# Performance work log

Measured on AMD Instinct MI355X. Metric: run time of the kernel, lower is better.

The kernel has to match this reference:

```python
import jax, jax.numpy as jnp
import numpy as np

N = 512   # speakers
M = 64    # samples per speaker
D = 768   # embedding dim
EPS = 1e-8  # torch F.cosine_similarity eps


def setup_inputs() -> dict:
    key = jax.random.key(0)
    k1, = jax.random.split(key, 1)
    speaker_vectors = jax.random.normal(k1, (N * M, D), dtype=jnp.float32)
    w = jnp.asarray(10.0, dtype=jnp.float32)
    b = jnp.asarray(-5.0, dtype=jnp.float32)
    return {"speaker_vectors": speaker_vectors, "w": w, "b": b}


def _cosine(a, b):
    # torch F.cosine_similarity: a.b / (max(|a|,eps) * max(|b|,eps)), over last dim
    na = jnp.maximum(jnp.linalg.norm(a, axis=-1), EPS)
    nb = jnp.maximum(jnp.linalg.norm(b, axis=-1), EPS)
    return jnp.sum(a * b, axis=-1) / (na * nb)


def reference(speaker_vectors, w, b):
    x = speaker_vectors.reshape(N, M, D)            # [N, M, D]
    sums = x.sum(axis=1)                            # [N, D]
    centroids = sums / M                            # [N, D]
    excl = (sums[:, None, :] - x) / (M - 1)         # exclusive centroids [N, M, D]

    # cosine sim of every centroid against every sample: [N_centroid, N_spk, M]
    xn = jnp.maximum(jnp.linalg.norm(x, axis=-1), EPS)          # [N, M]
    cn = jnp.maximum(jnp.linalg.norm(centroids, axis=-1), EPS)  # [N]
    dots = jnp.einsum('nd,imd->nim', centroids, x)              # [N, N, M]
    S = w * (dots / (cn[:, None, None] * xn[None])) + b         # [N, N, M]

    # same-speaker entries use the leave-one-out centroid
    S_same = w * _cosine(excl, x) + b               # [N, M]
    idx = jnp.arange(N)
    S = S.at[idx, idx].set(S_same)                  # overwrite diagonal block

    # L_j = -S_same_j + log sum_n exp(S[n, j])
    L = -S_same + jax.scipy.special.logsumexp(S, axis=0)  # [N, M]
    return L.sum()
```

## Files before the change

kernel.cpp:

```cpp
#include <hip/hip_runtime.h>
#include <hip/hip_bf16.h>
#include <math.h>

#define EPS 1e-8f

typedef __attribute__((ext_vector_type(2))) unsigned long ulongx2;
typedef __attribute__((ext_vector_type(4))) float floatx4;
typedef unsigned char uchar_t;

#define GPTR(p) ((const __attribute__((address_space(1))) void*)(p))
#define LPTR(p) ((__attribute__((address_space(3))) void*)(p))

__device__ __forceinline__ unsigned int pk4(float a, float b, float c, float d) {
  int v = __builtin_amdgcn_cvt_pk_fp8_f32(a, b, 0, false);
  v = __builtin_amdgcn_cvt_pk_fp8_f32(c, d, v, true);
  return (unsigned int)v;
}

__global__ __launch_bounds__(256) void kA(const float* __restrict__ x,
    uchar_t* __restrict__ xbf8fm, float* __restrict__ sums_f32,
    float* __restrict__ ss, float* __restrict__ rcn,
    float* __restrict__ xx, float* __restrict__ rxn,
    const float* __restrict__ wp) {
  const int n = blockIdx.x;
  const int t = threadIdx.x;
  const int wv = t >> 6, l = t & 63;
  __shared__ uchar_t xs[4][16][776];
  __shared__ float csum[4][768];
  float4 cs0 = {0,0,0,0}, cs1 = {0,0,0,0}, cs2 = {0,0,0,0};

  for (int r = 0; r < 16; ++r) {
    const int row = wv * 16 + r;
    const size_t base = ((size_t)n * 64 + row) * 768;
    const float* rp = x + base;
    float4 v0 = *(const float4*)(rp + l * 4);
    float4 v1 = *(const float4*)(rp + l * 4 + 256);
    float4 v2 = *(const float4*)(rp + l * 4 + 512);
    *(unsigned int*)&xs[wv][r][l * 4]       = pk4(v0.x, v0.y, v0.z, v0.w);
    *(unsigned int*)&xs[wv][r][l * 4 + 256] = pk4(v1.x, v1.y, v1.z, v1.w);
    *(unsigned int*)&xs[wv][r][l * 4 + 512] = pk4(v2.x, v2.y, v2.z, v2.w);
    float rq = v0.x*v0.x + v0.y*v0.y + v0.z*v0.z + v0.w*v0.w
             + v1.x*v1.x + v1.y*v1.y + v1.z*v1.z + v1.w*v1.w
             + v2.x*v2.x + v2.y*v2.y + v2.z*v2.z + v2.w*v2.w;
    for (int o = 32; o; o >>= 1) rq += __shfl_xor(rq, o, 64);
    if (l == 0) {
      const int j = n * 64 + row;
      xx[j] = rq;
      rxn[j] = 1.0f / fmaxf(sqrtf(rq), EPS);
    }
    cs0.x += v0.x; cs0.y += v0.y; cs0.z += v0.z; cs0.w += v0.w;
    cs1.x += v1.x; cs1.y += v1.y; cs1.z += v1.z; cs1.w += v1.w;
    cs2.x += v2.x; cs2.y += v2.y; cs2.z += v2.z; cs2.w += v2.w;
  }
  *(float4*)&csum[wv][l * 4]       = cs0;
  *(float4*)&csum[wv][l * 4 + 256] = cs1;
  *(float4*)&csum[wv][l * 4 + 512] = cs2;
  __syncthreads();

  float lss = 0.f;
#pragma unroll
  for (int q = 0; q < 3; ++q) {
    const int c = t + q * 256;
    const float s = csum[0][c] + csum[1][c] + csum[2][c] + csum[3][c];
    sums_f32[(size_t)n * 768 + c] = s;
    lss += s * s;
  }
  for (int o = 32; o; o >>= 1) lss += __shfl_xor(lss, o, 64);
  __syncthreads();
  if (l == 0) csum[1][wv] = lss;
  __syncthreads();
  if (t == 0) {
    const float v = csum[1][0] + csum[1][1] + csum[1][2] + csum[1][3];
    ss[n] = v;
    rcn[n] = (*wp) / fmaxf(sqrtf(v), 64.f * EPS);
  }

  {
    const int g = n * 4 + wv;
#pragma unroll
    for (int ks = 0; ks < 12; ++ks) {
      const uchar_t* sp = &xs[wv][l & 15][ks * 64 + (l >> 4) * 8];
      uint2 lo = *(const uint2*)sp;
      uint2 hi = *(const uint2*)(sp + 32);
      uint4 outv = {lo.x, lo.y, hi.x, hi.y};
      *(uint4*)(xbf8fm + (size_t)((g * 12 + ks) * 64 + l) * 16) = outv;
    }
  }
}

__global__ __launch_bounds__(256) void kA2(const float* __restrict__ sums_f32,
    uchar_t* __restrict__ sums8fm) {
  const int g = blockIdx.x;
  const int wv = threadIdx.x >> 6, l = threadIdx.x & 63;
#pragma unroll
  for (int ksi = 0; ksi < 3; ++ksi) {
    const int ks = wv * 3 + ksi;
    const float* sp = sums_f32 + (size_t)(g * 16 + (l & 15)) * 768
                      + ks * 64 + (l >> 4) * 8;
    float4 a0 = *(const float4*)sp;
    float4 a1 = *(const float4*)(sp + 4);
    float4 b0 = *(const float4*)(sp + 32);
    float4 b1 = *(const float4*)(sp + 36);
    uint4 outv = { pk4(a0.x, a0.y, a0.z, a0.w), pk4(a1.x, a1.y, a1.z, a1.w),
                   pk4(b0.x, b0.y, b0.z, b0.w), pk4(b1.x, b1.y, b1.z, b1.w) };
    *(uint4*)(sums8fm + (size_t)((g * 12 + ks) * 64 + l) * 16) = outv;
  }
}

__global__ __launch_bounds__(512, 2) void kC(const uchar_t* __restrict__ xbf8fm,
    const uchar_t* __restrict__ sums8fm, const float* __restrict__ rcn,
    const float* __restrict__ rxn, float* __restrict__ colsum,
    float* __restrict__ sdiag_dot, const float* __restrict__ bp) {
  __shared__ uchar_t lds[4][32768];
  const int b = blockIdx.x;
  const int xcd = b & 7;
  const int inner = b >> 3;
  const int nt = inner & 1;
  const int jt = xcd + ((inner >> 1) << 3);
  const int n0 = nt * 256, j0 = jt * 256;
  const int t = threadIdx.x, wv = t >> 6, l = t & 63;
  const int wm = wv >> 2, wj = wv & 3;
  const int gA0 = n0 / 16, gB0 = j0 / 16;

#define STAGE(KS_, BUF_) {                                                     \
    const int fb0_ = wv * 2, fb1_ = wv * 2 + 1;                                \
    __builtin_amdgcn_global_load_lds(                                          \
        GPTR(sums8fm + (size_t)(((gA0 + fb0_) * 12 + (KS_)) * 64 + l) * 16),   \
        LPTR(&lds[BUF_][fb0_ * 1024]), 16, 0, 0);                              \
    __builtin_amdgcn_global_load_lds(                                          \
        GPTR(sums8fm + (size_t)(((gA0 + fb1_) * 12 + (KS_)) * 64 + l) * 16),   \
        LPTR(&lds[BUF_][fb1_ * 1024]), 16, 0, 0);                              \
    __builtin_amdgcn_global_load_lds(                                          \
        GPTR(xbf8fm + (size_t)(((gB0 + fb0_) * 12 + (KS_)) * 64 + l) * 16),    \
        LPTR(&lds[BUF_][16384 + fb0_ * 1024]), 16, 0, 0);                      \
    __builtin_amdgcn_global_load_lds(                                          \
        GPTR(xbf8fm + (size_t)(((gB0 + fb1_) * 12 + (KS_)) * 64 + l) * 16),    \
        LPTR(&lds[BUF_][16384 + fb1_ * 1024]), 16, 0, 0);                      \
  }

  floatx4 acc[8][4];
#pragma unroll
  for (int mi = 0; mi < 8; ++mi)
#pragma unroll
    for (int ni = 0; ni < 4; ++ni) acc[mi][ni] = (floatx4){0.f, 0.f, 0.f, 0.f};

  STAGE(0, 0)
  STAGE(1, 1)
  STAGE(2, 2)

  for (int kb = 0; kb < 12; ++kb) {
    if (kb < 10)       { asm volatile("s_waitcnt vmcnt(8)" ::: "memory"); }
    else if (kb == 10) { asm volatile("s_waitcnt vmcnt(4)" ::: "memory"); }
    else               { asm volatile("s_waitcnt vmcnt(0)" ::: "memory"); }
    __builtin_amdgcn_s_barrier();
    __builtin_amdgcn_sched_barrier(0);
    const int cb = kb & 3, sb = (kb + 3) & 3;

    ulongx2 af[8], bf[4];
#pragma unroll
    for (int ni = 0; ni < 4; ++ni)
      bf[ni] = *(const ulongx2*)&lds[cb][16384 + (wj * 4 + ni) * 1024 + l * 16];
#pragma unroll
    for (int mi = 0; mi < 8; ++mi)
      af[mi] = *(const ulongx2*)&lds[cb][(wm * 8 + mi) * 1024 + l * 16];
    if (kb + 3 < 12) STAGE(kb + 3, sb)
    __builtin_amdgcn_s_setprio(1);
#pragma unroll
    for (int mi = 0; mi < 8; ++mi)
#pragma unroll
      for (int ni = 0; ni < 4; ++ni) {
        acc[mi][ni] = __builtin_amdgcn_mfma_f32_16x16x32_fp8_fp8(
            (long)af[mi].x, (long)bf[ni].x, acc[mi][ni], 0, 0, 0);
        acc[mi][ni] = __builtin_amdgcn_mfma_f32_16x16x32_fp8_fp8(
            (long)af[mi].y, (long)bf[ni].y, acc[mi][ni], 0, 0, 0);
      }
    __builtin_amdgcn_s_setprio(0);
  }

  const float bb = *bp;
  float rxv[4], p[4] = {0.f, 0.f, 0.f, 0.f};
#pragma unroll
  for (int ni = 0; ni < 4; ++ni)
    rxv[ni] = rxn[j0 + wj * 64 + ni * 16 + (l & 15)];
  const bool diagblk = (nt == (jt >> 6));

#pragma unroll
  for (int mi = 0; mi < 8; ++mi) {
    float4 rr = *(const float4*)&rcn[n0 + wm * 128 + mi * 16 + ((l >> 4) << 2)];
    const float rc[4] = {rr.x, rr.y, rr.z, rr.w};
#pragma unroll
    for (int ni = 0; ni < 4; ++ni) {
      floatx4 a = acc[mi][ni];
#pragma unroll
      for (int q = 0; q < 4; ++q)
        p[ni] += __expf(a[q] * rc[q] * rxv[ni] + bb);
      if (diagblk) {
        const int jg = j0 + wj * 64 + ni * 16 + (l & 15);
#pragma unroll
        for (int q = 0; q < 4; ++q) {
          const int mg = n0 + wm * 128 + mi * 16 + ((l >> 4) << 2) + q;
          if (mg == (jg >> 6)) sdiag_dot[jg] = a[q];
        }
      }
    }
  }
#pragma unroll
  for (int ni = 0; ni < 4; ++ni) {
    p[ni] += __shfl_xor(p[ni], 16, 64);
    p[ni] += __shfl_xor(p[ni], 32, 64);
  }
  if (l < 16) {
#pragma unroll
    for (int ni = 0; ni < 4; ++ni)
      atomicAdd(&colsum[j0 + wj * 64 + ni * 16 + l], p[ni]);
  }
}

__global__ __launch_bounds__(256) void kD(const float* __restrict__ colsum,
    const float* __restrict__ sdiag_dot, const float* __restrict__ xx,
    const float* __restrict__ ss, const float* __restrict__ rcn,
    const float* __restrict__ wp, const float* __restrict__ bp,
    float* __restrict__ out) {
  const int j = blockIdx.x * 256 + threadIdx.x;
  const int i = j >> 6;
  const float ww = *wp, bb = *bp;
  const float sx = sdiag_dot[j];
  const float xxv = xx[j];
  const float xn = fmaxf(sqrtf(xxv), EPS);
  const float rx = 1.0f / xn;
  const float sd = sx * rcn[i] * rx + bb;
  const float exn = sqrtf(fmaxf(ss[i] - 2.f * sx + xxv, 0.f)) * (1.f / 63.f);
  const float edot = (sx - xxv) * (1.f / 63.f);
  const float sm = ww * edot / (fmaxf(exn, EPS) * xn) + bb;
  const float tot = colsum[j] - __expf(sd) + __expf(sm);
  float L = -sm + logf(fmaxf(tot, 1e-30f));
  for (int o = 32; o; o >>= 1) L += __shfl_xor(L, o, 64);
  __shared__ float red[4];
  if ((threadIdx.x & 63) == 0) red[threadIdx.x >> 6] = L;
  __syncthreads();
  if (threadIdx.x == 0) atomicAdd(out, red[0] + red[1] + red[2] + red[3]);
}

extern "C" void kernel_launch(void* const* d_in, const int* in_sizes, int n_in,
                              void* d_out, int out_size, void* d_ws, size_t ws_size,
                              hipStream_t stream) {
  const float* x  = (const float*)d_in[0];
  const float* wp = (const float*)d_in[1];
  const float* bp = (const float*)d_in[2];
  float* out = (float*)d_out;

  float* fws = (float*)d_ws;
  float* ss        = fws;
  float* rcn       = fws + 512;
  float* xx        = fws + 1024;
  float* rxn       = fws + 33792;
  float* colsum    = fws + 66560;
  float* sdiag_dot = fws + 99328;
  float* sums_f32  = fws + 132096;
  uchar_t* sums8fm = (uchar_t*)(fws + 525312);
  uchar_t* xbf8fm  = (uchar_t*)(fws + 623616);

  hipMemsetAsync(colsum, 0, 32768 * sizeof(float), stream);
  hipMemsetAsync(out, 0, sizeof(float), stream);

  kA<<<512, 256, 0, stream>>>(x, xbf8fm, sums_f32, ss, rcn, xx, rxn, wp);
  kA2<<<32, 256, 0, stream>>>(sums_f32, sums8fm);
  kC<<<256, 512, 0, stream>>>(xbf8fm, sums8fm, rcn, rxn, colsum, sdiag_dot, bp);
  kD<<<128, 256, 0, stream>>>(colsum, sdiag_dot, xx, ss, rcn, wp, bp, out);
}
```

Before: 58.38 us.

## Split kA into 16-row blocks with atomic centroid sums; move norms to kA2

kA now launches one block per 16-sample group (2048 blocks) instead of one per speaker (512). Each block accumulates its partial speaker sums into a zeroed sums buffer with float atomics. The centroid squared-norm and scale computation moves into kA2, which now reads the completed sums. This is meant to raise occupancy and bandwidth use in the memory-bound conversion pass. The cost is an extra memset, 4-way atomic contention per element, and non-deterministic summation order.

```diff
diff --git a/kernel.cpp b/kernel.cpp
--- a/kernel.cpp
+++ b/kernel.cpp
@@ -19,32 +19,32 @@
 
 __global__ __launch_bounds__(256) void kA(const float* __restrict__ x,
     uchar_t* __restrict__ xbf8fm, float* __restrict__ sums_f32,
-    float* __restrict__ ss, float* __restrict__ rcn,
-    float* __restrict__ xx, float* __restrict__ rxn,
-    const float* __restrict__ wp) {
-  const int n = blockIdx.x;
+    float* __restrict__ xx, float* __restrict__ rxn) {
+  const int g = blockIdx.x;
+  const int n = g >> 2;
   const int t = threadIdx.x;
   const int wv = t >> 6, l = t & 63;
-  __shared__ uchar_t xs[4][16][776];
+  __shared__ uchar_t xs[16][776];
   __shared__ float csum[4][768];
   float4 cs0 = {0,0,0,0}, cs1 = {0,0,0,0}, cs2 = {0,0,0,0};
 
-  for (int r = 0; r < 16; ++r) {
-    const int row = wv * 16 + r;
-    const size_t base = ((size_t)n * 64 + row) * 768;
+#pragma unroll
+  for (int rr = 0; rr < 4; ++rr) {
+    const int r = wv * 4 + rr;
+    const size_t base = ((size_t)g * 16 + r) * 768;
     const float* rp = x + base;
     float4 v0 = *(const float4*)(rp + l * 4);
     float4 v1 = *(const float4*)(rp + l * 4 + 256);
     float4 v2 = *(const float4*)(rp + l * 4 + 512);
-    *(unsigned int*)&xs[wv][r][l * 4]       = pk4(v0.x, v0.y, v0.z, v0.w);
-    *(unsigned int*)&xs[wv][r][l * 4 + 256] = pk4(v1.x, v1.y, v1.z, v1.w);
-    *(unsigned int*)&xs[wv][r][l * 4 + 512] = pk4(v2.x, v2.y, v2.z, v2.w);
+    *(unsigned int*)&xs[r][l * 4]       = pk4(v0.x, v0.y, v0.z, v0.w);
+    *(unsigned int*)&xs[r][l * 4 + 256] = pk4(v1.x, v1.y, v1.z, v1.w);
+    *(unsigned int*)&xs[r][l * 4 + 512] = pk4(v2.x, v2.y, v2.z, v2.w);
     float rq = v0.x*v0.x + v0.y*v0.y + v0.z*v0.z + v0.w*v0.w
              + v1.x*v1.x + v1.y*v1.y + v1.z*v1.z + v1.w*v1.w
              + v2.x*v2.x + v2.y*v2.y + v2.z*v2.z + v2.w*v2.w;
     for (int o = 32; o; o >>= 1) rq += __shfl_xor(rq, o, 64);
     if (l == 0) {
-      const int j = n * 64 + row;
+      const int j = g * 16 + r;
       xx[j] = rq;
       rxn[j] = 1.0f / fmaxf(sqrtf(rq), EPS);
     }
@@ -57,39 +57,27 @@
   *(float4*)&csum[wv][l * 4 + 512] = cs2;
   __syncthreads();
 
-  float lss = 0.f;
 #pragma unroll
   for (int q = 0; q < 3; ++q) {
     const int c = t + q * 256;
     const float s = csum[0][c] + csum[1][c] + csum[2][c] + csum[3][c];
-    sums_f32[(size_t)n * 768 + c] = s;
-    lss += s * s;
-  }
-  for (int o = 32; o; o >>= 1) lss += __shfl_xor(lss, o, 64);
-  __syncthreads();
-  if (l == 0) csum[1][wv] = lss;
-  __syncthreads();
-  if (t == 0) {
-    const float v = csum[1][0] + csum[1][1] + csum[1][2] + csum[1][3];
-    ss[n] = v;
-    rcn[n] = (*wp) / fmaxf(sqrtf(v), 64.f * EPS);
-  }
-
-  {
-    const int g = n * 4 + wv;
-#pragma unroll
-    for (int ks = 0; ks < 12; ++ks) {
-      const uchar_t* sp = &xs[wv][l & 15][ks * 64 + (l >> 4) * 8];
-      uint2 lo = *(const uint2*)sp;
-      uint2 hi = *(const uint2*)(sp + 32);
-      uint4 outv = {lo.x, lo.y, hi.x, hi.y};
-      *(uint4*)(xbf8fm + (size_t)((g * 12 + ks) * 64 + l) * 16) = outv;
-    }
+    atomicAdd(&sums_f32[(size_t)n * 768 + c], s);
+  }
+
+#pragma unroll
+  for (int ksi = 0; ksi < 3; ++ksi) {
+    const int ks = wv * 3 + ksi;
+    const uchar_t* sp = &xs[l & 15][ks * 64 + (l >> 4) * 8];
+    uint2 lo = *(const uint2*)sp;
+    uint2 hi = *(const uint2*)(sp + 32);
+    uint4 outv = {lo.x, lo.y, hi.x, hi.y};
+    *(uint4*)(xbf8fm + (size_t)((g * 12 + ks) * 64 + l) * 16) = outv;
   }
 }
 
 __global__ __launch_bounds__(256) void kA2(const float* __restrict__ sums_f32,
-    uchar_t* __restrict__ sums8fm) {
+    uchar_t* __restrict__ sums8fm, float* __restrict__ ss,
+    float* __restrict__ rcn, const float* __restrict__ wp) {
   const int g = blockIdx.x;
   const int wv = threadIdx.x >> 6, l = threadIdx.x & 63;
 #pragma unroll
@@ -104,6 +92,22 @@
     uint4 outv = { pk4(a0.x, a0.y, a0.z, a0.w), pk4(a1.x, a1.y, a1.z, a1.w),
                    pk4(b0.x, b0.y, b0.z, b0.w), pk4(b1.x, b1.y, b1.z, b1.w) };
     *(uint4*)(sums8fm + (size_t)((g * 12 + ks) * 64 + l) * 16) = outv;
+  }
+#pragma unroll
+  for (int sp4 = 0; sp4 < 4; ++sp4) {
+    const int n = g * 16 + wv * 4 + sp4;
+    const float* spt = sums_f32 + (size_t)n * 768;
+    float4 u0 = *(const float4*)(spt + l * 4);
+    float4 u1 = *(const float4*)(spt + l * 4 + 256);
+    float4 u2 = *(const float4*)(spt + l * 4 + 512);
+    float lss = u0.x*u0.x + u0.y*u0.y + u0.z*u0.z + u0.w*u0.w
+              + u1.x*u1.x + u1.y*u1.y + u1.z*u1.z + u1.w*u1.w
+              + u2.x*u2.x + u2.y*u2.y + u2.z*u2.z + u2.w*u2.w;
+    for (int o = 32; o; o >>= 1) lss += __shfl_xor(lss, o, 64);
+    if (l == 0) {
+      ss[n] = lss;
+      rcn[n] = (*wp) / fmaxf(sqrtf(lss), 64.f * EPS);
+    }
   }
 }
 
@@ -261,10 +265,11 @@
   uchar_t* xbf8fm  = (uchar_t*)(fws + 623616);
 
   hipMemsetAsync(colsum, 0, 32768 * sizeof(float), stream);
+  hipMemsetAsync(sums_f32, 0, 393216 * sizeof(float), stream);
   hipMemsetAsync(out, 0, sizeof(float), stream);
 
-  kA<<<512, 256, 0, stream>>>(x, xbf8fm, sums_f32, ss, rcn, xx, rxn, wp);
-  kA2<<<32, 256, 0, stream>>>(sums_f32, sums8fm);
+  kA<<<2048, 256, 0, stream>>>(x, xbf8fm, sums_f32, xx, rxn);
+  kA2<<<32, 256, 0, stream>>>(sums_f32, sums8fm, ss, rcn, wp);
   kC<<<256, 512, 0, stream>>>(xbf8fm, sums8fm, rcn, rxn, colsum, sdiag_dot, bp);
   kD<<<128, 256, 0, stream>>>(colsum, sdiag_dot, xx, ss, rcn, wp, bp, out);
 }
```

Measured after the change: 63.21 us. +8.3%, slower.

## Replace atomics and memsets with partial-sum buffers and batch row loads in kA

Applied to the files above, without the earlier changes.

Column sums from kC are now written to four per-slot partial buffers instead of atomically accumulated, and kD sums those slots. kD writes per-block partials that a new single-block kE reduces. This removes both memset launches and all float atomics, and makes the result deterministic. In exchange it adds one kernel launch and a larger workspace. Separately, kA now issues loads for four rows at once before processing them, to raise memory-level parallelism.

```diff
diff --git a/kernel.cpp b/kernel.cpp
--- a/kernel.cpp
+++ b/kernel.cpp
@@ -27,34 +27,41 @@
   const int wv = t >> 6, l = t & 63;
   __shared__ uchar_t xs[4][16][776];
   __shared__ float csum[4][768];
-  float4 cs0 = {0,0,0,0}, cs1 = {0,0,0,0}, cs2 = {0,0,0,0};
-
-  for (int r = 0; r < 16; ++r) {
-    const int row = wv * 16 + r;
-    const size_t base = ((size_t)n * 64 + row) * 768;
-    const float* rp = x + base;
-    float4 v0 = *(const float4*)(rp + l * 4);
-    float4 v1 = *(const float4*)(rp + l * 4 + 256);
-    float4 v2 = *(const float4*)(rp + l * 4 + 512);
-    *(unsigned int*)&xs[wv][r][l * 4]       = pk4(v0.x, v0.y, v0.z, v0.w);
-    *(unsigned int*)&xs[wv][r][l * 4 + 256] = pk4(v1.x, v1.y, v1.z, v1.w);
-    *(unsigned int*)&xs[wv][r][l * 4 + 512] = pk4(v2.x, v2.y, v2.z, v2.w);
-    float rq = v0.x*v0.x + v0.y*v0.y + v0.z*v0.z + v0.w*v0.w
-             + v1.x*v1.x + v1.y*v1.y + v1.z*v1.z + v1.w*v1.w
-             + v2.x*v2.x + v2.y*v2.y + v2.z*v2.z + v2.w*v2.w;
-    for (int o = 32; o; o >>= 1) rq += __shfl_xor(rq, o, 64);
-    if (l == 0) {
-      const int j = n * 64 + row;
-      xx[j] = rq;
-      rxn[j] = 1.0f / fmaxf(sqrtf(rq), EPS);
-    }
-    cs0.x += v0.x; cs0.y += v0.y; cs0.z += v0.z; cs0.w += v0.w;
-    cs1.x += v1.x; cs1.y += v1.y; cs1.z += v1.z; cs1.w += v1.w;
-    cs2.x += v2.x; cs2.y += v2.y; cs2.z += v2.z; cs2.w += v2.w;
-  }
-  *(float4*)&csum[wv][l * 4]       = cs0;
-  *(float4*)&csum[wv][l * 4 + 256] = cs1;
-  *(float4*)&csum[wv][l * 4 + 512] = cs2;
+  float4 cs[3] = {{0,0,0,0},{0,0,0,0},{0,0,0,0}};
+
+  for (int c4 = 0; c4 < 4; ++c4) {
+    float4 v[4][3];
+#pragma unroll
+    for (int rr = 0; rr < 4; ++rr) {
+      const int r = wv * 16 + c4 * 4 + rr;
+      const float* rp = x + ((size_t)n * 64 + r) * 768 + l * 4;
+#pragma unroll
+      for (int q = 0; q < 3; ++q) v[rr][q] = *(const float4*)(rp + q * 256);
+    }
+#pragma unroll
+    for (int rr = 0; rr < 4; ++rr) {
+      const int r = c4 * 4 + rr;
+      float rq = 0.f;
+#pragma unroll
+      for (int q = 0; q < 3; ++q) {
+        const float4 u = v[rr][q];
+        *(unsigned int*)&xs[wv][r][l * 4 + q * 256] = pk4(u.x, u.y, u.z, u.w);
+        rq += u.x*u.x + u.y*u.y + u.z*u.z + u.w*u.w;
+        cs[q].x += u.x; cs[q].y += u.y; cs[q].z += u.z; cs[q].w += u.w;
+      }
+      for (int o = 32; o; o >>= 1) rq += __shfl_xor(rq, o, 64);
+      if (l == 0) {
+        const int j = n * 64 + wv * 16 + r - wv * 16 + wv * 16;
+        const int jj = n * 64 + wv * 16 + c4 * 4 + rr;
+        xx[jj] = rq;
+        rxn[jj] = 1.0f / fmaxf(sqrtf(rq), EPS);
+        (void)j;
+      }
+    }
+  }
+#pragma unroll
+  for (int q = 0; q < 3; ++q)
+    *(float4*)&csum[wv][l * 4 + q * 256] = cs[q];
   __syncthreads();
 
   float lss = 0.f;
@@ -70,9 +77,9 @@
   if (l == 0) csum[1][wv] = lss;
   __syncthreads();
   if (t == 0) {
-    const float v = csum[1][0] + csum[1][1] + csum[1][2] + csum[1][3];
-    ss[n] = v;
-    rcn[n] = (*wp) / fmaxf(sqrtf(v), 64.f * EPS);
+    const float vv = csum[1][0] + csum[1][1] + csum[1][2] + csum[1][3];
+    ss[n] = vv;
+    rcn[n] = (*wp) / fmaxf(sqrtf(vv), 64.f * EPS);
   }
 
   {
@@ -109,7 +116,7 @@
 
 __global__ __launch_bounds__(512, 2) void kC(const uchar_t* __restrict__ xbf8fm,
     const uchar_t* __restrict__ sums8fm, const float* __restrict__ rcn,
-    const float* __restrict__ rxn, float* __restrict__ colsum,
+    const float* __restrict__ rxn, float* __restrict__ colsum_part,
     float* __restrict__ sdiag_dot, const float* __restrict__ bp) {
   __shared__ uchar_t lds[4][32768];
   const int b = blockIdx.x;
@@ -210,17 +217,18 @@
     p[ni] += __shfl_xor(p[ni], 32, 64);
   }
   if (l < 16) {
+    const int slot = nt * 2 + wm;
 #pragma unroll
     for (int ni = 0; ni < 4; ++ni)
-      atomicAdd(&colsum[j0 + wj * 64 + ni * 16 + l], p[ni]);
-  }
-}
-
-__global__ __launch_bounds__(256) void kD(const float* __restrict__ colsum,
+      colsum_part[(size_t)slot * 32768 + j0 + wj * 64 + ni * 16 + l] = p[ni];
+  }
+}
+
+__global__ __launch_bounds__(256) void kD(const float* __restrict__ colsum_part,
     const float* __restrict__ sdiag_dot, const float* __restrict__ xx,
     const float* __restrict__ ss, const float* __restrict__ rcn,
     const float* __restrict__ wp, const float* __restrict__ bp,
-    float* __restrict__ out) {
+    float* __restrict__ partial) {
   const int j = blockIdx.x * 256 + threadIdx.x;
   const int i = j >> 6;
   const float ww = *wp, bb = *bp;
@@ -232,13 +240,27 @@
   const float exn = sqrtf(fmaxf(ss[i] - 2.f * sx + xxv, 0.f)) * (1.f / 63.f);
   const float edot = (sx - xxv) * (1.f / 63.f);
   const float sm = ww * edot / (fmaxf(exn, EPS) * xn) + bb;
-  const float tot = colsum[j] - __expf(sd) + __expf(sm);
+  const float cssum = colsum_part[j] + colsum_part[32768 + j]
+                    + colsum_part[65536 + j] + colsum_part[98304 + j];
+  const float tot = cssum - __expf(sd) + __expf(sm);
   float L = -sm + logf(fmaxf(tot, 1e-30f));
   for (int o = 32; o; o >>= 1) L += __shfl_xor(L, o, 64);
   __shared__ float red[4];
   if ((threadIdx.x & 63) == 0) red[threadIdx.x >> 6] = L;
   __syncthreads();
-  if (threadIdx.x == 0) atomicAdd(out, red[0] + red[1] + red[2] + red[3]);
+  if (threadIdx.x == 0)
+    partial[blockIdx.x] = red[0] + red[1] + red[2] + red[3];
+}
+
+__global__ __launch_bounds__(128) void kE(const float* __restrict__ partial,
+    float* __restrict__ out) {
+  const int t = threadIdx.x;
+  float v = partial[t];
+  for (int o = 32; o; o >>= 1) v += __shfl_xor(v, o, 64);
+  __shared__ float r2[2];
+  if ((t & 63) == 0) r2[t >> 6] = v;
+  __syncthreads();
+  if (t == 0) out[0] = r2[0] + r2[1];
 }
 
 extern "C" void kernel_launch(void* const* d_in, const int* in_sizes, int n_in,
@@ -250,21 +272,20 @@
   float* out = (float*)d_out;
 
   float* fws = (float*)d_ws;
-  float* ss        = fws;
-  float* rcn       = fws + 512;
-  float* xx        = fws + 1024;
-  float* rxn       = fws + 33792;
-  float* colsum    = fws + 66560;
-  float* sdiag_dot = fws + 99328;
-  float* sums_f32  = fws + 132096;
-  uchar_t* sums8fm = (uchar_t*)(fws + 525312);
-  uchar_t* xbf8fm  = (uchar_t*)(fws + 623616);
-
-  hipMemsetAsync(colsum, 0, 32768 * sizeof(float), stream);
-  hipMemsetAsync(out, 0, sizeof(float), stream);
+  float* ss          = fws;
+  float* rcn         = fws + 512;
+  float* xx          = fws + 1024;
+  float* rxn         = fws + 33792;
+  float* colsum_part = fws + 66560;
+  float* sdiag_dot   = fws + 197632;
+  float* partial     = fws + 230400;
+  float* sums_f32    = fws + 230528;
+  uchar_t* sums8fm   = (uchar_t*)(fws + 623744);
+  uchar_t* xbf8fm    = (uchar_t*)(fws + 722048);
 
   kA<<<512, 256, 0, stream>>>(x, xbf8fm, sums_f32, ss, rcn, xx, rxn, wp);
   kA2<<<32, 256, 0, stream>>>(sums_f32, sums8fm);
-  kC<<<256, 512, 0, stream>>>(xbf8fm, sums8fm, rcn, rxn, colsum, sdiag_dot, bp);
-  kD<<<128, 256, 0, stream>>>(colsum, sdiag_dot, xx, ss, rcn, wp, bp, out);
-}
+  kC<<<256, 512, 0, stream>>>(xbf8fm, sums8fm, rcn, rxn, colsum_part, sdiag_dot, bp);
+  kD<<<128, 256, 0, stream>>>(colsum_part, sdiag_dot, xx, ss, rcn, wp, bp, partial);
+  kE<<<1, 128, 0, stream>>>(partial, out);
+}
```

Result: faster. 52.61 us (-9.9%).
